# Kernel tuning notes

Measured on AMD Instinct MI355X. Metric: run time of the kernel, lower is better.

Reference implementation:

```python
import jax, jax.numpy as jnp
import numpy as np

B, D, L = 16384, 2048, 6

def setup_inputs() -> dict:
    key = jax.random.key(0)
    kx, kw = jax.random.split(key)
    x = jax.random.normal(kx, (B, D), dtype=jnp.float32)
    # cross weights: xavier_normal on (D,1) -> std = sqrt(2/(D+1)); stacked [L, D]
    std = float(np.sqrt(2.0 / (D + 1)))
    W = jax.random.normal(kw, (L, D), dtype=jnp.float32) * std
    b = jnp.zeros((L, D), dtype=jnp.float32)  # bias params init to zeros
    return {"x": x, "W": W, "b": b}

def reference(x, W, b):
    # Original per layer: x_l = (x0 @ x_l^T) @ w_i + b_i + x_l
    # Algebraically identical: x_l = x0 * (x_l . w_i) + b_i + x_l  (scalar per row)
    x_l = x
    for i in range(W.shape[0]):
        s = jnp.einsum('bd,d->b', x_l, W[i])          # [B]
        x_l = x * s[:, None] + b[i][None, :] + x_l     # [B, D]
    return x_l
```

## Files before the change

### kernel.cpp

```cpp
#include <hip/hip_runtime.h>

#define B_ROWS   16384
#define D_DIM    2048
#define L_LAYERS 6
#define THREADS  256
#define BLOCKS   1024

__global__ __launch_bounds__(THREADS) void cross_net_kernel(
    const float* __restrict__ x,
    const float* __restrict__ W,
    const float* __restrict__ b,
    float* __restrict__ out)
{
    const int t    = threadIdx.x;
    const int lane = t & 63;
    const int wid  = t >> 6;
    const int base0 = t * 4;
    const int base1 = 1024 + t * 4;

    __shared__ float s_part[4][L_LAYERS];

    float w[L_LAYERS][8];
    float prefix[8];
    float e_red[L_LAYERS];
    #pragma unroll
    for (int j = 0; j < 8; ++j) prefix[j] = 0.f;
    #pragma unroll
    for (int l = 0; l < L_LAYERS; ++l) e_red[l] = 0.f;

    #pragma unroll
    for (int l = 0; l < L_LAYERS; ++l) {
        const float4 w0 = *(const float4*)(W + l * D_DIM + base0);
        const float4 w1 = *(const float4*)(W + l * D_DIM + base1);
        w[l][0] = w0.x; w[l][1] = w0.y; w[l][2] = w0.z; w[l][3] = w0.w;
        w[l][4] = w1.x; w[l][5] = w1.y; w[l][6] = w1.z; w[l][7] = w1.w;
        const float4 b0 = *(const float4*)(b + l * D_DIM + base0);
        const float4 b1 = *(const float4*)(b + l * D_DIM + base1);
        const float bl[8] = {b0.x, b0.y, b0.z, b0.w, b1.x, b1.y, b1.z, b1.w};
        #pragma unroll
        for (int j = 0; j < 8; ++j) {
            e_red[l] += prefix[j] * w[l][j];
            prefix[j] += bl[j];
        }
    }
    float U[8];
    #pragma unroll
    for (int j = 0; j < 8; ++j) U[j] = prefix[j];

    #pragma unroll
    for (int l = 0; l < L_LAYERS; ++l) {
        float v = e_red[l];
        #pragma unroll
        for (int off = 32; off >= 1; off >>= 1) v += __shfl_xor(v, off, 64);
        e_red[l] = v;
    }
    if (lane == 0) {
        #pragma unroll
        for (int l = 0; l < L_LAYERS; ++l) s_part[wid][l] = e_red[l];
    }
    __syncthreads();
    float e[L_LAYERS];
    #pragma unroll
    for (int l = 0; l < L_LAYERS; ++l)
        e[l] = s_part[0][l] + s_part[1][l] + s_part[2][l] + s_part[3][l];
    __syncthreads();

    const int rows_per_block = B_ROWS / BLOCKS;
    const int row0 = blockIdx.x * rows_per_block;
    for (int r = 0; r < rows_per_block; ++r) {
        const int row = row0 + r;
        const float* xr = x + (size_t)row * D_DIM;
        const float4 x0 = *(const float4*)(xr + base0);
        const float4 x1 = *(const float4*)(xr + base1);
        const float xv[8] = {x0.x, x0.y, x0.z, x0.w, x1.x, x1.y, x1.z, x1.w};

        float p[L_LAYERS];
        #pragma unroll
        for (int l = 0; l < L_LAYERS; ++l) {
            float acc = 0.f;
            #pragma unroll
            for (int j = 0; j < 8; ++j) acc += xv[j] * w[l][j];
            p[l] = acc;
        }
        #pragma unroll
        for (int l = 0; l < L_LAYERS; ++l) {
            #pragma unroll
            for (int off = 32; off >= 1; off >>= 1) p[l] += __shfl_xor(p[l], off, 64);
        }
        if (lane == 0) {
            #pragma unroll
            for (int l = 0; l < L_LAYERS; ++l) s_part[wid][l] = p[l];
        }
        __syncthreads();

        float c = 1.f;
        #pragma unroll
        for (int l = 0; l < L_LAYERS; ++l) {
            const float dsum = s_part[0][l] + s_part[1][l] + s_part[2][l] + s_part[3][l];
            c = c * (1.f + dsum) + e[l];
        }

        float* orow = out + (size_t)row * D_DIM;
        float4 o0, o1;
        o0.x = c * xv[0] + U[0]; o0.y = c * xv[1] + U[1];
        o0.z = c * xv[2] + U[2]; o0.w = c * xv[3] + U[3];
        o1.x = c * xv[4] + U[4]; o1.y = c * xv[5] + U[5];
        o1.z = c * xv[6] + U[6]; o1.w = c * xv[7] + U[7];
        *(float4*)(orow + base0) = o0;
        *(float4*)(orow + base1) = o1;

        __syncthreads();
    }
}

extern "C" void kernel_launch(void* const* d_in, const int* in_sizes, int n_in,
                              void* d_out, int out_size, void* d_ws, size_t ws_size,
                              hipStream_t stream) {
    (void)in_sizes; (void)n_in; (void)d_ws; (void)ws_size; (void)out_size;
    const float* x = (const float*)d_in[0];
    const float* W = (const float*)d_in[1];
    const float* b = (const float*)d_in[2];
    float* out = (float*)d_out;
    cross_net_kernel<<<dim3(BLOCKS), dim3(THREADS), 0, stream>>>(x, W, b, out);
}
```

Baseline: 250.1 us.

## Assign rows per wavefront with shared-memory weights to remove block barriers

Work is now split so that each 64-lane wavefront handles two full rows, instead of a whole 256-thread block handling each row. The cross-layer weights and the bias prefix are staged once into LDS. Per-row reductions now happen only through wave shuffles, which removes the two __syncthreads per row and the serialized row loop. All loads for both rows are issued up front for memory-level parallelism. In exchange, register use goes up (16 float4 of x per thread), LDS use goes up to about 56KB per block, and there is a one-time staging cost per block.

After: 308.2 us. 1.23x slower.

```diff
diff --git a/kernel.cpp b/kernel.cpp
--- a/kernel.cpp
+++ b/kernel.cpp
@@ -3,113 +3,111 @@
 #define B_ROWS   16384
 #define D_DIM    2048
 #define L_LAYERS 6
-#define THREADS  256
+#define THREADS  512
 #define BLOCKS   1024
+#define WPB      (THREADS / 64)
+#define ROWS_PER_WAVE 2
 
-__global__ __launch_bounds__(THREADS) void cross_net_kernel(
+__global__ __launch_bounds__(THREADS, 4) void cross_net_kernel(
     const float* __restrict__ x,
     const float* __restrict__ W,
     const float* __restrict__ b,
     float* __restrict__ out)
 {
+    __shared__ float Wl[L_LAYERS][D_DIM];
+    __shared__ float Ul[D_DIM];
+    __shared__ float red[WPB][L_LAYERS];
+
     const int t    = threadIdx.x;
     const int lane = t & 63;
     const int wid  = t >> 6;
-    const int base0 = t * 4;
-    const int base1 = 1024 + t * 4;
 
-    __shared__ float s_part[4][L_LAYERS];
+    {
+        const int base = t * 4;
+        float4 prefix = make_float4(0.f, 0.f, 0.f, 0.f);
+        float e_red[L_LAYERS];
+        #pragma unroll
+        for (int l = 0; l < L_LAYERS; ++l) {
+            const float4 wv = *(const float4*)(W + l * D_DIM + base);
+            const float4 bv = *(const float4*)(b + l * D_DIM + base);
+            e_red[l] = prefix.x * wv.x + prefix.y * wv.y +
+                       prefix.z * wv.z + prefix.w * wv.w;
+            prefix.x += bv.x; prefix.y += bv.y; prefix.z += bv.z; prefix.w += bv.w;
+            *(float4*)&Wl[l][base] = wv;
+        }
+        *(float4*)&Ul[base] = prefix;
+        #pragma unroll
+        for (int l = 0; l < L_LAYERS; ++l) {
+            float v = e_red[l];
+            #pragma unroll
+            for (int off = 32; off >= 1; off >>= 1) v += __shfl_xor(v, off, 64);
+            if (lane == 0) red[wid][l] = v;
+        }
+    }
+    __syncthreads();
 
-    float w[L_LAYERS][8];
-    float prefix[8];
-    float e_red[L_LAYERS];
+    float e[L_LAYERS];
     #pragma unroll
-    for (int j = 0; j < 8; ++j) prefix[j] = 0.f;
+    for (int l = 0; l < L_LAYERS; ++l) {
+        float s = 0.f;
+        #pragma unroll
+        for (int w = 0; w < WPB; ++w) s += red[w][l];
+        e[l] = s;
+    }
+
+    const int gw   = blockIdx.x * WPB + wid;
+    const int row0 = gw * ROWS_PER_WAVE;
+    const float* xr0 = x + (size_t)row0 * D_DIM;
+    const float* xr1 = xr0 + D_DIM;
+    const int eoff = lane * 4;
+
+    float4 xa[8], xb[8];
     #pragma unroll
-    for (int l = 0; l < L_LAYERS; ++l) e_red[l] = 0.f;
+    for (int j = 0; j < 8; ++j) xa[j] = *(const float4*)(xr0 + j * 256 + eoff);
+    #pragma unroll
+    for (int j = 0; j < 8; ++j) xb[j] = *(const float4*)(xr1 + j * 256 + eoff);
+
+    float p0[L_LAYERS], p1[L_LAYERS];
+    #pragma unroll
+    for (int l = 0; l < L_LAYERS; ++l) {
+        float a0 = 0.f, a1 = 0.f;
+        #pragma unroll
+        for (int j = 0; j < 8; ++j) {
+            const float4 wv = *(const float4*)&Wl[l][j * 256 + eoff];
+            a0 += xa[j].x * wv.x + xa[j].y * wv.y + xa[j].z * wv.z + xa[j].w * wv.w;
+            a1 += xb[j].x * wv.x + xb[j].y * wv.y + xb[j].z * wv.z + xb[j].w * wv.w;
+        }
+        p0[l] = a0; p1[l] = a1;
+    }
 
     #pragma unroll
-    for (int l = 0; l < L_LAYERS; ++l) {
-        const float4 w0 = *(const float4*)(W + l * D_DIM + base0);
-        const float4 w1 = *(const float4*)(W + l * D_DIM + base1);
-        w[l][0] = w0.x; w[l][1] = w0.y; w[l][2] = w0.z; w[l][3] = w0.w;
-        w[l][4] = w1.x; w[l][5] = w1.y; w[l][6] = w1.z; w[l][7] = w1.w;
-        const float4 b0 = *(const float4*)(b + l * D_DIM + base0);
-        const float4 b1 = *(const float4*)(b + l * D_DIM + base1);
-        const float bl[8] = {b0.x, b0.y, b0.z, b0.w, b1.x, b1.y, b1.z, b1.w};
+    for (int off = 32; off >= 1; off >>= 1) {
         #pragma unroll
-        for (int j = 0; j < 8; ++j) {
-            e_red[l] += prefix[j] * w[l][j];
-            prefix[j] += bl[j];
+        for (int l = 0; l < L_LAYERS; ++l) {
+            p0[l] += __shfl_xor(p0[l], off, 64);
+            p1[l] += __shfl_xor(p1[l], off, 64);
         }
     }
-    float U[8];
-    #pragma unroll
-    for (int j = 0; j < 8; ++j) U[j] = prefix[j];
 
+    float c0 = 1.f, c1 = 1.f;
     #pragma unroll
     for (int l = 0; l < L_LAYERS; ++l) {
-        float v = e_red[l];
-        #pragma unroll
-        for (int off = 32; off >= 1; off >>= 1) v += __shfl_xor(v, off, 64);
-        e_red[l] = v;
+        c0 = c0 * (1.f + p0[l]) + e[l];
+        c1 = c1 * (1.f + p1[l]) + e[l];
     }
-    if (lane == 0) {
-        #pragma unroll
-        for (int l = 0; l < L_LAYERS; ++l) s_part[wid][l] = e_red[l];
-    }
-    __syncthreads();
-    float e[L_LAYERS];
+
+    float* or0 = out + (size_t)row0 * D_DIM;
+    float* or1 = or0 + D_DIM;
     #pragma unroll
-    for (int l = 0; l < L_LAYERS; ++l)
-        e[l] = s_part[0][l] + s_part[1][l] + s_part[2][l] + s_part[3][l];
-    __syncthreads();
-
-    const int rows_per_block = B_ROWS / BLOCKS;
-    const int row0 = blockIdx.x * rows_per_block;
-    for (int r = 0; r < rows_per_block; ++r) {
-        const int row = row0 + r;
-        const float* xr = x + (size_t)row * D_DIM;
-        const float4 x0 = *(const float4*)(xr + base0);
-        const float4 x1 = *(const float4*)(xr + base1);
-        const float xv[8] = {x0.x, x0.y, x0.z, x0.w, x1.x, x1.y, x1.z, x1.w};
-
-        float p[L_LAYERS];
-        #pragma unroll
-        for (int l = 0; l < L_LAYERS; ++l) {
-            float acc = 0.f;
-            #pragma unroll
-            for (int j = 0; j < 8; ++j) acc += xv[j] * w[l][j];
-            p[l] = acc;
-        }
-        #pragma unroll
-        for (int l = 0; l < L_LAYERS; ++l) {
-            #pragma unroll
-            for (int off = 32; off >= 1; off >>= 1) p[l] += __shfl_xor(p[l], off, 64);
-        }
-        if (lane == 0) {
-            #pragma unroll
-            for (int l = 0; l < L_LAYERS; ++l) s_part[wid][l] = p[l];
-        }
-        __syncthreads();
-
-        float c = 1.f;
-        #pragma unroll
-        for (int l = 0; l < L_LAYERS; ++l) {
-            const float dsum = s_part[0][l] + s_part[1][l] + s_part[2][l] + s_part[3][l];
-            c = c * (1.f + dsum) + e[l];
-        }
-
-        float* orow = out + (size_t)row * D_DIM;
+    for (int j = 0; j < 8; ++j) {
+        const float4 uv = *(const float4*)&Ul[j * 256 + eoff];
         float4 o0, o1;
-        o0.x = c * xv[0] + U[0]; o0.y = c * xv[1] + U[1];
-        o0.z = c * xv[2] + U[2]; o0.w = c * xv[3] + U[3];
-        o1.x = c * xv[4] + U[4]; o1.y = c * xv[5] + U[5];
-        o1.z = c * xv[6] + U[6]; o1.w = c * xv[7] + U[7];
-        *(float4*)(orow + base0) = o0;
-        *(float4*)(orow + base1) = o1;
-
-        __syncthreads();
+        o0.x = c0 * xa[j].x + uv.x; o0.y = c0 * xa[j].y + uv.y;
+        o0.z = c0 * xa[j].z + uv.z; o0.w = c0 * xa[j].w + uv.w;
+        o1.x = c1 * xb[j].x + uv.x; o1.y = c1 * xb[j].y + uv.y;
+        o1.z = c1 * xb[j].z + uv.z; o1.w = c1 * xb[j].w + uv.w;
+        *(float4*)(or0 + j * 256 + eoff) = o0;
+        *(float4*)(or1 + j * 256 + eoff) = o1;
     }
 }
 
```
